# Optimization experiments

Hardware: AMD Instinct MI355X
Metric: run time of the kernel (lower is better)

The kernel has to match this reference:

```python
import jax, jax.numpy as jnp
import numpy as np

FILTER_WIDTH = 6


def setup_inputs() -> dict:
    key = jax.random.key(0)
    ks = jax.random.split(key, 9)
    V, E, H, C = 50000, 128, 128, 2
    B, S = 64, 512
    inputs = jax.random.randint(ks[0], (B, S), 0, V)
    lengths = jax.random.randint(ks[1], (B,), 1, S)
    embed_table = (jax.random.normal(ks[2], (V, E), jnp.float32) * 0.1).at[0].set(0.0)  # padding_idx=0
    s = 1.0 / np.sqrt(H)
    w_ih = jax.random.uniform(ks[3], (4 * H, E), jnp.float32, -s, s)
    w_hh = jax.random.uniform(ks[4], (4 * H, H), jnp.float32, -s, s)
    b_ih = jax.random.uniform(ks[5], (4 * H,), jnp.float32, -s, s)
    b_hh = jax.random.uniform(ks[6], (4 * H,), jnp.float32, -s, s)
    sf = 1.0 / np.sqrt(H)
    fc_w = jax.random.uniform(ks[7], (C, H), jnp.float32, -sf, sf)
    fc_b = jax.random.uniform(ks[8], (C,), jnp.float32, -sf, sf)
    return dict(inputs=inputs, lengths=lengths, embed_table=embed_table,
                w_ih=w_ih, w_hh=w_hh, b_ih=b_ih, b_hh=b_hh, fc_w=fc_w, fc_b=fc_b)


def reference(inputs, lengths, embed_table, w_ih, w_hh, b_ih, b_hh, fc_w, fc_b):
    # Dropouts are identity in eval mode (p set to 0).
    B, S = inputs.shape
    E = embed_table.shape[1]
    H = w_hh.shape[1]
    FW = FILTER_WIDTH
    W = S - FW + 1

    emb = embed_table[inputs]                                   # [B, S, E]
    idx = jnp.arange(W)[:, None] + jnp.arange(FW)[None, :]       # [W, FW]
    xw = emb[:, idx, :]                                          # [B, W, FW, E] sliding windows
    x = xw.reshape(B * W, FW, E).transpose(1, 0, 2)              # [FW, B*W, E] time-major

    bias = b_ih + b_hh

    def step(carry, xt):
        h, c = carry
        g = xt @ w_ih.T + h @ w_hh.T + bias                      # [B*W, 4H], gate order i,f,g,o
        i, f, gg, o = jnp.split(g, 4, axis=-1)
        c = jax.nn.sigmoid(f) * c + jax.nn.sigmoid(i) * jnp.tanh(gg)
        h = jax.nn.sigmoid(o) * jnp.tanh(c)
        return (h, c), None

    h0 = jnp.zeros((B * W, H), emb.dtype)
    (h_last, _), _ = jax.lax.scan(step, (h0, h0), x)             # final hidden per window
    feat = jnp.max(h_last.reshape(B, W, H), axis=1)              # max-pool over windows
    return feat @ fc_w.T + fc_b                                  # [B, num_class]
```

## Files before the change

kernel.cpp:

```cpp
#include <hip/hip_runtime.h>
#include <math.h>
#include <float.h>

#define Bn   64
#define Sn   512
#define FWn  6
#define Wn   507
#define WT   32
#define NTILE 16

#define PROWS   37
#define PSTRIDE 516

typedef __attribute__((ext_vector_type(8))) _Float16 half8;
typedef __attribute__((ext_vector_type(4))) _Float16 half4;
typedef __attribute__((ext_vector_type(4))) float f32x4;

__device__ __forceinline__ float sigf(float x)  {
    return __builtin_amdgcn_rcpf(1.0f + __expf(-x));
}
__device__ __forceinline__ float tanh_(float x) {
    return 1.0f - 2.0f * __builtin_amdgcn_rcpf(__expf(2.0f * x) + 1.0f);
}

__global__ void __launch_bounds__(256)
pack_w_kernel(const float* __restrict__ w_ih, const float* __restrict__ w_hh,
              _Float16* __restrict__ wih_p, _Float16* __restrict__ whh_p)
{
    const int idx = blockIdx.x * 256 + threadIdx.x;
    const int j  = idx & 7;
    const int L  = (idx >> 3) & 63;
    const int ks = (idx >> 9) & 3;
    const int nt = idx >> 11;
    const int row = nt * 16 + (L & 15);
    const int col = ks * 32 + (L >> 4) * 8 + j;
    wih_p[idx] = (_Float16)w_ih[row * 128 + col];
    whh_p[idx] = (_Float16)w_hh[row * 128 + col];
}

__global__ void __launch_bounds__(512)
lstm_kernel(const int* __restrict__ inputs, const float* __restrict__ embed,
            const _Float16* __restrict__ wih_p, const _Float16* __restrict__ whh_p,
            const float* __restrict__ b_ih, const float* __restrict__ b_hh,
            float* __restrict__ partial)
{
    __shared__ __align__(16) _Float16 Pt[PROWS * PSTRIDE];
    __shared__ __align__(16) _Float16 hsA[2][2][2048];
    const int t    = threadIdx.x;
    const int L    = t & 63;
    const int ut   = t >> 6;
    const int b    = blockIdx.x >> 4;
    const int tile = blockIdx.x & 15;
    const int w0   = tile * WT;
    const int q  = L >> 4;
    const int ln = L & 15;
    const int j8 = L & 7;
    const int u  = ut * 16 + ln;

    {
        f32x4 accx[3][4];
#pragma unroll
        for (int g = 0; g < 4; ++g) {
            const float bg = b_ih[g * 128 + u] + b_hh[g * 128 + u];
            accx[0][g] = (f32x4){bg, bg, bg, bg};
            accx[1][g] = accx[0][g];
            accx[2][g] = accx[0][g];
        }
        int tok[3];
#pragma unroll
        for (int mt = 0; mt < 3; ++mt) {
            int s = w0 + mt * 16 + ln; s = s < 511 ? s : 511;
            tok[mt] = inputs[b * Sn + s];
        }
#pragma unroll
        for (int ks = 0; ks < 4; ++ks) {
            half8 ax[3];
#pragma unroll
            for (int mt = 0; mt < 3; ++mt) {
                const float* er = embed + (size_t)tok[mt] * 128 + ks * 32 + q * 8;
                float4 e0 = *(const float4*)er;
                float4 e1 = *(const float4*)(er + 4);
                half8 a;
                a[0] = (_Float16)e0.x; a[1] = (_Float16)e0.y;
                a[2] = (_Float16)e0.z; a[3] = (_Float16)e0.w;
                a[4] = (_Float16)e1.x; a[5] = (_Float16)e1.y;
                a[6] = (_Float16)e1.z; a[7] = (_Float16)e1.w;
                ax[mt] = a;
            }
#pragma unroll
            for (int g = 0; g < 4; ++g) {
                half8 bw = *(const half8*)(wih_p + ((size_t)((g * 8 + ut) * 4 + ks) * 64 + L) * 8);
#pragma unroll
                for (int mt = 0; mt < 3; ++mt)
                    accx[mt][g] = __builtin_amdgcn_mfma_f32_16x16x32_f16(ax[mt], bw, accx[mt][g], 0, 0, 0);
            }
        }
#pragma unroll
        for (int mt = 0; mt < 3; ++mt)
#pragma unroll
            for (int r = 0; r < 4; ++r) {
                const int sl = mt * 16 + q * 4 + r;
                if (sl < PROWS) {
                    half4 o;
                    o[0] = (_Float16)accx[mt][0][r];
                    o[1] = (_Float16)accx[mt][1][r];
                    o[2] = (_Float16)accx[mt][2][r];
                    o[3] = (_Float16)accx[mt][3][r];
                    *(half4*)&Pt[sl * PSTRIDE + u * 4] = o;
                }
            }
    }

    half8 whf[4][4];
#pragma unroll
    for (int g = 0; g < 4; ++g)
#pragma unroll
        for (int ks = 0; ks < 4; ++ks)
            whf[g][ks] = *(const half8*)(whh_p + ((size_t)((g * 8 + ut) * 4 + ks) * 64 + L) * 8);

    __syncthreads();

    const int ks_h = ut >> 1;
    const int qp   = (ut & 1) * 2 + (ln >> 3);

    float cst[2][4] = {{0.f, 0.f, 0.f, 0.f}, {0.f, 0.f, 0.f, 0.f}};
    float hh[2][4];

    for (int st = 0; st < FWn; ++st) {
        if (st > 0) __syncthreads();
#pragma unroll
        for (int sub = 0; sub < 2; ++sub) {
            f32x4 acc[4];
#pragma unroll
            for (int r = 0; r < 4; ++r) {
                half4 pv = *(const half4*)&Pt[(sub * 16 + q * 4 + r + st) * PSTRIDE + u * 4];
                acc[0][r] = (float)pv[0]; acc[1][r] = (float)pv[1];
                acc[2][r] = (float)pv[2]; acc[3][r] = (float)pv[3];
            }
            if (st > 0) {
                const _Float16* hb = hsA[(st + 1) & 1][sub];
#pragma unroll
                for (int ks = 0; ks < 4; ++ks) {
                    half8 ah = *(const half8*)(hb + (ks * 64 + L) * 8);
#pragma unroll
                    for (int g = 0; g < 4; ++g)
                        acc[g] = __builtin_amdgcn_mfma_f32_16x16x32_f16(ah, whf[g][ks], acc[g], 0, 0, 0);
                }
            }
            _Float16* buf = hsA[st & 1][sub];
#pragma unroll
            for (int r = 0; r < 4; ++r) {
                float ii = sigf(acc[0][r]);
                float ff = sigf(acc[1][r]);
                float gg = tanh_(acc[2][r]);
                float oo = sigf(acc[3][r]);
                float cc = ff * cst[sub][r] + ii * gg;
                cst[sub][r] = cc;
                hh[sub][r] = oo * tanh_(cc);
                if (st < FWn - 1)
                    buf[ks_h * 512 + (qp * 16 + q * 4 + r) * 8 + j8] = (_Float16)hh[sub][r];
            }
        }
    }

    float mv = -FLT_MAX;
#pragma unroll
    for (int sub = 0; sub < 2; ++sub)
#pragma unroll
        for (int r = 0; r < 4; ++r) {
            const int w = w0 + sub * 16 + q * 4 + r;
            if (w < Wn) mv = fmaxf(mv, hh[sub][r]);
        }
    mv = fmaxf(mv, __shfl_xor(mv, 16));
    mv = fmaxf(mv, __shfl_xor(mv, 32));
    if (q == 0)
        partial[(size_t)(b * NTILE + tile) * 128 + u] = mv;
}

__global__ void __launch_bounds__(128)
final_kernel(const float* __restrict__ partial, const float* __restrict__ fc_w,
             const float* __restrict__ fc_b, float* __restrict__ out)
{
    const int b = blockIdx.x;
    const int u = threadIdx.x;
    float m = -FLT_MAX;
#pragma unroll
    for (int tl = 0; tl < NTILE; ++tl)
        m = fmaxf(m, partial[(size_t)(b * NTILE + tl) * 128 + u]);
    float v0 = m * fc_w[u];
    float v1 = m * fc_w[128 + u];
#pragma unroll
    for (int off = 1; off < 64; off <<= 1) {
        v0 += __shfl_xor(v0, off);
        v1 += __shfl_xor(v1, off);
    }
    __shared__ float red[2][2];
    if ((u & 63) == 0) { red[u >> 6][0] = v0; red[u >> 6][1] = v1; }
    __syncthreads();
    if (u == 0) {
        out[b * 2 + 0] = red[0][0] + red[1][0] + fc_b[0];
        out[b * 2 + 1] = red[0][1] + red[1][1] + fc_b[1];
    }
}

extern "C" void kernel_launch(void* const* d_in, const int* in_sizes, int n_in,
                              void* d_out, int out_size, void* d_ws, size_t ws_size,
                              hipStream_t stream)
{
    const int*   inputs = (const int*)d_in[0];
    const float* embed  = (const float*)d_in[2];
    const float* w_ih   = (const float*)d_in[3];
    const float* w_hh   = (const float*)d_in[4];
    const float* b_ih   = (const float*)d_in[5];
    const float* b_hh   = (const float*)d_in[6];
    const float* fc_w   = (const float*)d_in[7];
    const float* fc_b   = (const float*)d_in[8];
    float* out = (float*)d_out;

    float*    partial = (float*)d_ws;
    _Float16* wih_p   = (_Float16*)(partial + Bn * NTILE * 128);
    _Float16* whh_p   = wih_p + 65536;

    pack_w_kernel<<<dim3(256), 256, 0, stream>>>(w_ih, w_hh, wih_p, whh_p);
    lstm_kernel<<<dim3(Bn * NTILE), 512, 0, stream>>>(inputs, embed, wih_p, whh_p,
                                                      b_ih, b_hh, partial);
    final_kernel<<<dim3(Bn), 128, 0, stream>>>(partial, fc_w, fc_b, out);
}
```

Measured before the change: 140.3 us.

## Widen window tile to 48 and batch recurrent MFMAs across sub-tiles

```diff
diff --git a/kernel.cpp b/kernel.cpp
--- a/kernel.cpp
+++ b/kernel.cpp
@@ -6,10 +6,10 @@
 #define Sn   512
 #define FWn  6
 #define Wn   507
-#define WT   32
-#define NTILE 16
-
-#define PROWS   37
+#define WT   48
+#define NTILE 11
+
+#define PROWS   53
 #define PSTRIDE 516
 
 typedef __attribute__((ext_vector_type(8))) _Float16 half8;
@@ -45,12 +45,12 @@
             float* __restrict__ partial)
 {
     __shared__ __align__(16) _Float16 Pt[PROWS * PSTRIDE];
-    __shared__ __align__(16) _Float16 hsA[2][2][2048];
+    __shared__ __align__(16) _Float16 hsA[2][3][2048];
     const int t    = threadIdx.x;
     const int L    = t & 63;
     const int ut   = t >> 6;
-    const int b    = blockIdx.x >> 4;
-    const int tile = blockIdx.x & 15;
+    const int b    = blockIdx.x / NTILE;
+    const int tile = blockIdx.x % NTILE;
     const int w0   = tile * WT;
     const int q  = L >> 4;
     const int ln = L & 15;
@@ -58,25 +58,26 @@
     const int u  = ut * 16 + ln;
 
     {
-        f32x4 accx[3][4];
+        f32x4 accx[4][4];
 #pragma unroll
         for (int g = 0; g < 4; ++g) {
             const float bg = b_ih[g * 128 + u] + b_hh[g * 128 + u];
             accx[0][g] = (f32x4){bg, bg, bg, bg};
             accx[1][g] = accx[0][g];
             accx[2][g] = accx[0][g];
-        }
-        int tok[3];
-#pragma unroll
-        for (int mt = 0; mt < 3; ++mt) {
+            accx[3][g] = accx[0][g];
+        }
+        int tok[4];
+#pragma unroll
+        for (int mt = 0; mt < 4; ++mt) {
             int s = w0 + mt * 16 + ln; s = s < 511 ? s : 511;
             tok[mt] = inputs[b * Sn + s];
         }
 #pragma unroll
         for (int ks = 0; ks < 4; ++ks) {
-            half8 ax[3];
-#pragma unroll
-            for (int mt = 0; mt < 3; ++mt) {
+            half8 ax[4];
+#pragma unroll
+            for (int mt = 0; mt < 4; ++mt) {
                 const float* er = embed + (size_t)tok[mt] * 128 + ks * 32 + q * 8;
                 float4 e0 = *(const float4*)er;
                 float4 e1 = *(const float4*)(er + 4);
@@ -91,12 +92,12 @@
             for (int g = 0; g < 4; ++g) {
                 half8 bw = *(const half8*)(wih_p + ((size_t)((g * 8 + ut) * 4 + ks) * 64 + L) * 8);
 #pragma unroll
-                for (int mt = 0; mt < 3; ++mt)
+                for (int mt = 0; mt < 4; ++mt)
                     accx[mt][g] = __builtin_amdgcn_mfma_f32_16x16x32_f16(ax[mt], bw, accx[mt][g], 0, 0, 0);
             }
         }
 #pragma unroll
-        for (int mt = 0; mt < 3; ++mt)
+        for (int mt = 0; mt < 4; ++mt)
 #pragma unroll
             for (int r = 0; r < 4; ++r) {
                 const int sl = mt * 16 + q * 4 + r;
@@ -123,37 +124,42 @@
     const int ks_h = ut >> 1;
     const int qp   = (ut & 1) * 2 + (ln >> 3);
 
-    float cst[2][4] = {{0.f, 0.f, 0.f, 0.f}, {0.f, 0.f, 0.f, 0.f}};
-    float hh[2][4];
+    float cst[3][4] = {{0.f,0.f,0.f,0.f}, {0.f,0.f,0.f,0.f}, {0.f,0.f,0.f,0.f}};
+    float hh[3][4];
 
     for (int st = 0; st < FWn; ++st) {
-        if (st > 0) __syncthreads();
-#pragma unroll
-        for (int sub = 0; sub < 2; ++sub) {
-            f32x4 acc[4];
+        f32x4 acc[3][4];
+#pragma unroll
+        for (int sub = 0; sub < 3; ++sub)
 #pragma unroll
             for (int r = 0; r < 4; ++r) {
                 half4 pv = *(const half4*)&Pt[(sub * 16 + q * 4 + r + st) * PSTRIDE + u * 4];
-                acc[0][r] = (float)pv[0]; acc[1][r] = (float)pv[1];
-                acc[2][r] = (float)pv[2]; acc[3][r] = (float)pv[3];
-            }
-            if (st > 0) {
+                acc[sub][0][r] = (float)pv[0]; acc[sub][1][r] = (float)pv[1];
+                acc[sub][2][r] = (float)pv[2]; acc[sub][3][r] = (float)pv[3];
+            }
+        if (st > 0) {
+            __syncthreads();
+#pragma unroll
+            for (int sub = 0; sub < 3; ++sub) {
                 const _Float16* hb = hsA[(st + 1) & 1][sub];
 #pragma unroll
                 for (int ks = 0; ks < 4; ++ks) {
                     half8 ah = *(const half8*)(hb + (ks * 64 + L) * 8);
 #pragma unroll
                     for (int g = 0; g < 4; ++g)
-                        acc[g] = __builtin_amdgcn_mfma_f32_16x16x32_f16(ah, whf[g][ks], acc[g], 0, 0, 0);
+                        acc[sub][g] = __builtin_amdgcn_mfma_f32_16x16x32_f16(ah, whf[g][ks], acc[sub][g], 0, 0, 0);
                 }
             }
+        }
+#pragma unroll
+        for (int sub = 0; sub < 3; ++sub) {
             _Float16* buf = hsA[st & 1][sub];
 #pragma unroll
             for (int r = 0; r < 4; ++r) {
-                float ii = sigf(acc[0][r]);
-                float ff = sigf(acc[1][r]);
-                float gg = tanh_(acc[2][r]);
-                float oo = sigf(acc[3][r]);
+                float ii = sigf(acc[sub][0][r]);
+                float ff = sigf(acc[sub][1][r]);
+                float gg = tanh_(acc[sub][2][r]);
+                float oo = sigf(acc[sub][3][r]);
                 float cc = ff * cst[sub][r] + ii * gg;
                 cst[sub][r] = cc;
                 hh[sub][r] = oo * tanh_(cc);
@@ -165,7 +171,7 @@
 
     float mv = -FLT_MAX;
 #pragma unroll
-    for (int sub = 0; sub < 2; ++sub)
+    for (int sub = 0; sub < 3; ++sub)
 #pragma unroll
         for (int r = 0; r < 4; ++r) {
             const int w = w0 + sub * 16 + q * 4 + r;
```

New measurement: 156.5 us. 11.5% more time.
